# Optimization experiments

Hardware: AMD Instinct MI355X
Metric: run time of the kernel (lower is better)

## Reference

```python
import jax, jax.numpy as jnp
import numpy as np

H = 16          # num_heads
MAX_SCALE_MUL = float(np.log(100.0))
EPS = 1e-12     # F.normalize eps


def setup_inputs() -> dict:
    key = jax.random.key(0)
    ks = jax.random.split(key, 8)
    B, L, C = 8, 1024, 1024
    x = jax.random.normal(ks[0], (B, L, C), dtype=jnp.float32)
    attn_bias = jax.random.normal(ks[1], (1, H, L, L), dtype=jnp.float32) * 0.1
    w_qkv = jax.random.normal(ks[2], (3 * C, C), dtype=jnp.float32) * (C ** -0.5)
    q_bias = jnp.zeros((C,), dtype=jnp.float32)
    v_bias = jnp.zeros((C,), dtype=jnp.float32)
    scale_mul = jnp.full((1, H, 1, 1), np.log(4.0), dtype=jnp.float32)
    w_proj = jax.random.normal(ks[3], (C, C), dtype=jnp.float32) * (C ** -0.5)
    b_proj = jnp.zeros((C,), dtype=jnp.float32)
    return dict(x=x, attn_bias=attn_bias, w_qkv=w_qkv, q_bias=q_bias,
                v_bias=v_bias, scale_mul=scale_mul, w_proj=w_proj, b_proj=b_proj)


def _l2norm(t):
    # matches F.normalize(dim=-1): t / max(||t||_2, eps)
    n = jnp.sqrt(jnp.sum(t * t, axis=-1, keepdims=True))
    return t / jnp.maximum(n, EPS)


def reference(x, attn_bias, w_qkv, q_bias, v_bias, scale_mul, w_proj, b_proj):
    B, L, C = x.shape
    D = C // H
    bias = jnp.concatenate([q_bias, jnp.zeros_like(q_bias), v_bias])
    qkv = x @ w_qkv.T + bias                      # [B,L,3C]
    qkv = qkv.reshape(B, L, 3, H, D).transpose(2, 0, 3, 1, 4)  # [3,B,H,L,D]
    q, k, v = qkv[0], qkv[1], qkv[2]
    sm = jnp.exp(jnp.minimum(scale_mul, MAX_SCALE_MUL))        # [1,H,1,1]
    q = _l2norm(q) * sm
    k = _l2norm(k)
    attn = jnp.einsum('bhld,bhmd->bhlm', q, k) + attn_bias     # scale == 1
    attn = jax.nn.softmax(attn, axis=-1)
    out = jnp.einsum('bhlm,bhmd->bhld', attn, v)               # [B,H,L,D]
    out = out.transpose(0, 2, 1, 3).reshape(B, L, C)
    return out @ w_proj.T + b_proj
```

## Files before the change

### kernel.cpp

```cpp
#include <hip/hip_runtime.h>
#include <hip/hip_bf16.h>


#define LN100 4.6051701859880914f

typedef __attribute__((ext_vector_type(8))) short short8;
typedef __attribute__((ext_vector_type(4))) short short4v;
typedef __attribute__((ext_vector_type(4))) float f32x4;

#define MFMA_BF16(a, b, c) __builtin_amdgcn_mfma_f32_16x16x32_bf16(a, b, c, 0, 0, 0)

__device__ __forceinline__ unsigned short f2bf(float f) {
  unsigned u = __float_as_uint(f);
  u += 0x7fffu + ((u >> 16) & 1u);
  return (unsigned short)(u >> 16);
}
__device__ __forceinline__ float bf2f(unsigned short h) {
  return __uint_as_float(((unsigned)h) << 16);
}
__device__ __forceinline__ unsigned int pkbf2(float a, float b) {
  union { __hip_bfloat162 t; unsigned int u; } c;
  c.t = __float22bfloat162_rn(make_float2(a, b));
  return c.u;
}

__device__ __forceinline__ float bias_sel0(const float* qb, const float* vb, int col) {
  if (col < 1024) return qb[col];
  if (col < 2048) return 0.0f;
  return vb[col - 2048];
}

#define G2L16(gp, lp) __builtin_amdgcn_global_load_lds( \
    (const __attribute__((address_space(1))) void*)(gp), \
    (__attribute__((address_space(3))) void*)(lp), 16, 0, 0)

__global__ __launch_bounds__(256)
void split_f32_bf16(const float* __restrict__ in, unsigned short* __restrict__ hi,
                    unsigned short* __restrict__ lo, int n4)
{
  int i = blockIdx.x * blockDim.x + threadIdx.x;
  if (i >= n4) return;
  float4 v = ((const float4*)in)[i];
  ushort4 h, l;
  h.x = f2bf(v.x); l.x = f2bf(v.x - bf2f(h.x));
  h.y = f2bf(v.y); l.y = f2bf(v.y - bf2f(h.y));
  h.z = f2bf(v.z); l.z = f2bf(v.z - bf2f(h.z));
  h.w = f2bf(v.w); l.w = f2bf(v.w - bf2f(h.w));
  ((ushort4*)hi)[i] = h;
  ((ushort4*)lo)[i] = l;
}

template <int MODE>
__global__ __launch_bounds__(256)
void gemm_nt_split(const unsigned short* __restrict__ Ah, const unsigned short* __restrict__ Al,
                   const unsigned short* __restrict__ Wh, const unsigned short* __restrict__ Wl,
                   const float* __restrict__ b0, const float* __restrict__ b1,
                   float* __restrict__ C,
                   unsigned short* __restrict__ vth, unsigned short* __restrict__ vtl,
                   int M, int N, int K)
{
  __shared__ unsigned short sA[128 * 64];
  __shared__ unsigned short sW[128 * 64];

  const int tid  = threadIdx.x;
  const int lane = tid & 63;
  const int l15  = lane & 15, lg = lane >> 4;
  const int w    = tid >> 6;
  const int wr   = (w >> 1) << 6;
  const int wc   = (w & 1) << 6;
  const int m0   = blockIdx.y << 7;
  const int n0   = blockIdx.x << 7;

  f32x4 acc[4][4];
  #pragma unroll
  for (int i = 0; i < 4; ++i)
    #pragma unroll
    for (int j = 0; j < 4; ++j)
      acc[i][j] = (f32x4){0.f, 0.f, 0.f, 0.f};

  for (int k0 = 0; k0 < K; k0 += 32) {
    __syncthreads();
    #pragma unroll
    for (int u = 0; u < 4; ++u) {
      int idx = (u << 8) + tid;
      int row = idx >> 3;
      int c   = idx & 7;
      int s   = c ^ (row & 7);
      size_t rbA = (size_t)(m0 + row) * K + k0;
      size_t rbW = (size_t)(n0 + row) * K + k0;
      const unsigned short* srcA = (s < 4) ? (Ah + rbA + (s << 3))
                                           : (Al + rbA + ((s - 4) << 3));
      const unsigned short* srcW = (s < 4) ? (Wh + rbW + (s << 3))
                                           : (Wl + rbW + ((s - 4) << 3));
      G2L16(srcA, sA + (idx << 3));
      G2L16(srcW, sW + (idx << 3));
    }
    __syncthreads();

    short8 ah[4], al[4];
    #pragma unroll
    for (int i = 0; i < 4; ++i) {
      int row = wr + (i << 4) + l15;
      ah[i] = *(const short8*)(sA + (row << 6) + ((lg       ^ (row & 7)) << 3));
      al[i] = *(const short8*)(sA + (row << 6) + (((4 + lg) ^ (row & 7)) << 3));
    }
    #pragma unroll
    for (int j = 0; j < 4; ++j) {
      int row = wc + (j << 4) + l15;
      short8 wh = *(const short8*)(sW + (row << 6) + ((lg       ^ (row & 7)) << 3));
      short8 wl = *(const short8*)(sW + (row << 6) + (((4 + lg) ^ (row & 7)) << 3));
      #pragma unroll
      for (int i = 0; i < 4; ++i) {
        acc[i][j] = MFMA_BF16(ah[i], wh, acc[i][j]);
        acc[i][j] = MFMA_BF16(ah[i], wl, acc[i][j]);
        acc[i][j] = MFMA_BF16(al[i], wh, acc[i][j]);
      }
    }
  }

  if (MODE == 0 && n0 >= 2048) {
    #pragma unroll
    for (int j = 0; j < 4; ++j) {
      int col = n0 + wc + (j << 4) + l15;
      int d   = col - 2048;
      int hh  = d >> 6, dd = d & 63;
      float bb = b1[d];
      #pragma unroll
      for (int i = 0; i < 4; ++i) {
        int row  = m0 + wr + (i << 4) + (lg << 2);
        int bidx = row >> 10;
        int l    = row & 1023;
        size_t obase = ((((size_t)bidx << 4) + hh) << 6) + dd;
        obase = obase * 1024 + l;
        ushort4 hv, lv;
        float v0 = acc[i][j][0] + bb;
        float v1 = acc[i][j][1] + bb;
        float v2 = acc[i][j][2] + bb;
        float v3 = acc[i][j][3] + bb;
        hv.x = f2bf(v0); lv.x = f2bf(v0 - bf2f(hv.x));
        hv.y = f2bf(v1); lv.y = f2bf(v1 - bf2f(hv.y));
        hv.z = f2bf(v2); lv.z = f2bf(v2 - bf2f(hv.z));
        hv.w = f2bf(v3); lv.w = f2bf(v3 - bf2f(hv.w));
        *(ushort4*)(vth + obase) = hv;
        *(ushort4*)(vtl + obase) = lv;
      }
    }
  } else {
    #pragma unroll
    for (int j = 0; j < 4; ++j) {
      int col = n0 + wc + (j << 4) + l15;
      float bb = (MODE == 1) ? b0[col] : bias_sel0(b0, b1, col);
      #pragma unroll
      for (int i = 0; i < 4; ++i) {
        int rbase = m0 + wr + (i << 4) + (lg << 2);
        #pragma unroll
        for (int r = 0; r < 4; ++r)
          C[(size_t)(rbase + r) * N + col] = acc[i][j][r] + bb;
      }
    }
  }
}

__global__ __launch_bounds__(256)
void qk_norm_split(const float* __restrict__ qkv, const float* __restrict__ scale_mul,
                   unsigned short* __restrict__ qk_h, unsigned short* __restrict__ qk_l)
{
  int wave = (blockIdx.x << 2) + (threadIdx.x >> 6);
  int lane = threadIdx.x & 63;
  int h  = wave & 15;
  int bl = wave >> 4;
  size_t base = (size_t)bl * 3072 + (h << 6) + lane;
  float q = qkv[base];
  float k = qkv[base + 1024];
  float sq = q * q, sk = k * k;
  #pragma unroll
  for (int off = 32; off; off >>= 1) {
    sq += __shfl_xor(sq, off);
    sk += __shfl_xor(sk, off);
  }
  float sm = __expf(fminf(scale_mul[h], LN100));
  q = q / fmaxf(sqrtf(sq), 1e-12f) * sm;
  k = k / fmaxf(sqrtf(sk), 1e-12f);
  size_t ob = (size_t)bl * 2048 + (h << 6) + lane;
  unsigned short qh = f2bf(q);
  qk_h[ob] = qh;          qk_l[ob] = f2bf(q - bf2f(qh));
  unsigned short kh = f2bf(k);
  qk_h[ob + 1024] = kh;   qk_l[ob + 1024] = f2bf(k - bf2f(kh));
}

__global__ __launch_bounds__(256, 2)
void attn_mfma(const unsigned short* __restrict__ qk_h, const unsigned short* __restrict__ qk_l,
               const unsigned short* __restrict__ vth, const unsigned short* __restrict__ vtl,
               const float* __restrict__ bias,
               unsigned short* __restrict__ oh, unsigned short* __restrict__ ol)
{
  __shared__ unsigned short sKh[4096], sKl[4096];
  __shared__ unsigned short sVh[4096], sVl[4096];

  const int tid  = threadIdx.x;
  const int lane = tid & 63;
  const int l15  = lane & 15, lg = lane >> 4;
  const int w    = tid >> 6;
  const int qt = blockIdx.x & 7;
  const int h  = (blockIdx.x >> 3) & 15;
  const int b  = blockIdx.x >> 7;
  const int q0 = qt << 7;

  short8 qh[2][2], qlo[2][2];
  #pragma unroll
  for (int qf = 0; qf < 2; ++qf) {
    size_t rb = ((size_t)((b << 10) + q0 + (w << 5) + (qf << 4) + l15)) * 2048
              + (h << 6) + (lg << 3);
    qh[qf][0]  = *(const short8*)(qk_h + rb);
    qh[qf][1]  = *(const short8*)(qk_h + rb + 32);
    qlo[qf][0] = *(const short8*)(qk_l + rb);
    qlo[qf][1] = *(const short8*)(qk_l + rb + 32);
  }

  f32x4 ao[2][4];
  float mr[2], lr[2];
  #pragma unroll
  for (int qf = 0; qf < 2; ++qf) {
    #pragma unroll
    for (int j = 0; j < 4; ++j) ao[qf][j] = (f32x4){0.f, 0.f, 0.f, 0.f};
    mr[qf] = -3.0e38f; lr[qf] = 0.0f;
  }

  const unsigned short* kh_base = qk_h + 1024 + (h << 6);
  const unsigned short* kl_base = qk_l + 1024 + (h << 6);
  const size_t vbase = ((size_t)((b << 4) + h)) * 65536;
  const float* bias_base = bias + ((size_t)h << 20)
                         + (size_t)(q0 + (w << 5) + l15) * 1024 + (lg << 2);

  for (int kv0 = 0; kv0 < 1024; kv0 += 64) {
    __syncthreads();
    #pragma unroll
    for (int u = 0; u < 2; ++u) {
      int idx = (u << 8) + tid;
      int r = idx >> 3, c = idx & 7;
      int s = c ^ (r & 7);
      size_t krow = (size_t)((b << 10) + kv0 + r) * 2048 + (s << 3);
      size_t vrow = vbase + (size_t)r * 1024 + kv0 + (s << 3);
      G2L16(kh_base + krow, sKh + (idx << 3));
      G2L16(kl_base + krow, sKl + (idx << 3));
      G2L16(vth + vrow,     sVh + (idx << 3));
      G2L16(vtl + vrow,     sVl + (idx << 3));
    }
    float4 bb[2][4];
    #pragma unroll
    for (int qf = 0; qf < 2; ++qf)
      #pragma unroll
      for (int j = 0; j < 4; ++j)
        bb[qf][j] = *(const float4*)(bias_base + (size_t)(qf << 4) * 1024
                                     + kv0 + (j << 4));
    __syncthreads();

    f32x4 sv[2][4];
    #pragma unroll
    for (int j = 0; j < 4; ++j) {
      int row = (j << 4) + l15;
      int c0 = lg ^ (row & 7);
      int c1 = (lg + 4) ^ (row & 7);
      short8 kh0 = *(const short8*)(sKh + (row << 6) + (c0 << 3));
      short8 kl0 = *(const short8*)(sKl + (row << 6) + (c0 << 3));
      short8 kh1 = *(const short8*)(sKh + (row << 6) + (c1 << 3));
      short8 kl1 = *(const short8*)(sKl + (row << 6) + (c1 << 3));
      #pragma unroll
      for (int qf = 0; qf < 2; ++qf) {
        f32x4 a = (f32x4){0.f, 0.f, 0.f, 0.f};
        a = MFMA_BF16(kh0, qh[qf][0], a);
        a = MFMA_BF16(kl0, qh[qf][0], a);
        a = MFMA_BF16(kh0, qlo[qf][0], a);
        a = MFMA_BF16(kh1, qh[qf][1], a);
        a = MFMA_BF16(kl1, qh[qf][1], a);
        a = MFMA_BF16(kh1, qlo[qf][1], a);
        sv[qf][j] = a;
      }
    }

    unsigned int phw[2][8], plw[2][8];
    #pragma unroll
    for (int qf = 0; qf < 2; ++qf) {
      #pragma unroll
      for (int j = 0; j < 4; ++j) {
        sv[qf][j][0] += bb[qf][j].x;
        sv[qf][j][1] += bb[qf][j].y;
        sv[qf][j][2] += bb[qf][j].z;
        sv[qf][j][3] += bb[qf][j].w;
      }
      float mx = -3.0e38f;
      #pragma unroll
      for (int j = 0; j < 4; ++j)
        #pragma unroll
        for (int r = 0; r < 4; ++r) mx = fmaxf(mx, sv[qf][j][r]);
      mx = fmaxf(mx, __shfl_xor(mx, 16));
      mx = fmaxf(mx, __shfl_xor(mx, 32));
      float mn = fmaxf(mr[qf], mx);
      float al = __expf(mr[qf] - mn);
      mr[qf] = mn;
      float rs = 0.0f;
      #pragma unroll
      for (int j = 0; j < 4; ++j)
        #pragma unroll
        for (int r = 0; r < 4; ++r) {
          float e = __expf(sv[qf][j][r] - mn);
          sv[qf][j][r] = e;
          rs += e;
        }
      rs += __shfl_xor(rs, 16);
      rs += __shfl_xor(rs, 32);
      lr[qf] = lr[qf] * al + rs;
      #pragma unroll
      for (int r = 0; r < 4; ++r) {
        float av = __shfl(al, (lg << 2) + r);
        #pragma unroll
        for (int jd = 0; jd < 4; ++jd) ao[qf][jd][r] *= av;
      }
      #pragma unroll
      for (int j = 0; j < 4; ++j) {
        unsigned int h0 = pkbf2(sv[qf][j][0], sv[qf][j][1]);
        unsigned int h1 = pkbf2(sv[qf][j][2], sv[qf][j][3]);
        float r0 = sv[qf][j][0] - __uint_as_float(h0 << 16);
        float r1 = sv[qf][j][1] - __uint_as_float(h0 & 0xffff0000u);
        float r2 = sv[qf][j][2] - __uint_as_float(h1 << 16);
        float r3 = sv[qf][j][3] - __uint_as_float(h1 & 0xffff0000u);
        phw[qf][(j << 1)]     = h0;
        phw[qf][(j << 1) + 1] = h1;
        plw[qf][(j << 1)]     = pkbf2(r0, r1);
        plw[qf][(j << 1) + 1] = pkbf2(r2, r3);
      }
    }

    #pragma unroll
    for (int ks = 0; ks < 2; ++ks) {
      union { unsigned int w[4]; short8 v; } pa0, pa1, pl0, pl1;
      #pragma unroll
      for (int i = 0; i < 4; ++i) {
        pa0.w[i] = phw[0][(ks << 2) + i];
        pa1.w[i] = phw[1][(ks << 2) + i];
        pl0.w[i] = plw[0][(ks << 2) + i];
        pl1.w[i] = plw[1][(ks << 2) + i];
      }
      #pragma unroll
      for (int jd = 0; jd < 4; ++jd) {
        int vr  = (jd << 4) + l15;
        int c0  = ((ks << 2) + (lg >> 1))     ^ (vr & 7);
        int c1  = ((ks << 2) + 2 + (lg >> 1)) ^ (vr & 7);
        int sub = (lg & 1) << 2;
        short8 vh, vl;
        vh.lo = *(const short4v*)(sVh + (vr << 6) + (c0 << 3) + sub);
        vh.hi = *(const short4v*)(sVh + (vr << 6) + (c1 << 3) + sub);
        vl.lo = *(const short4v*)(sVl + (vr << 6) + (c0 << 3) + sub);
        vl.hi = *(const short4v*)(sVl + (vr << 6) + (c1 << 3) + sub);
        ao[0][jd] = MFMA_BF16(pa0.v, vh, ao[0][jd]);
        ao[0][jd] = MFMA_BF16(pa0.v, vl, ao[0][jd]);
        ao[0][jd] = MFMA_BF16(pl0.v, vh, ao[0][jd]);
        ao[1][jd] = MFMA_BF16(pa1.v, vh, ao[1][jd]);
        ao[1][jd] = MFMA_BF16(pa1.v, vl, ao[1][jd]);
        ao[1][jd] = MFMA_BF16(pl1.v, vh, ao[1][jd]);
      }
    }
  }

  #pragma unroll
  for (int qf = 0; qf < 2; ++qf)
    #pragma unroll
    for (int r = 0; r < 4; ++r) {
      float lv  = __shfl(lr[qf], (lg << 2) + r);
      float inv = 1.0f / lv;
      size_t orow = ((size_t)((b << 10) + q0 + (w << 5) + (qf << 4) + (lg << 2) + r)) * 1024
                  + (h << 6) + l15;
      #pragma unroll
      for (int jd = 0; jd < 4; ++jd) {
        float v = ao[qf][jd][r] * inv;
        unsigned short hb = f2bf(v);
        oh[orow + (jd << 4)] = hb;
        ol[orow + (jd << 4)] = f2bf(v - bf2f(hb));
      }
    }
}

template <int MODE>
__global__ __launch_bounds__(256)
void gemm_nt(const float* __restrict__ A, const float* __restrict__ Bw,
             const float* __restrict__ b0, const float* __restrict__ b1,
             float* __restrict__ C, int M, int N, int K)
{
  __shared__ float As[32][132];
  __shared__ float Bs[32][132];
  const int tid = threadIdx.x;
  const int tx = tid & 15, ty = tid >> 4;
  const int m0 = blockIdx.y << 7;
  const int n0 = blockIdx.x << 7;

  float acc[8][8];
  #pragma unroll
  for (int i = 0; i < 8; ++i)
    #pragma unroll
    for (int j = 0; j < 8; ++j) acc[i][j] = 0.0f;

  for (int k0 = 0; k0 < K; k0 += 32) {
    #pragma unroll
    for (int u = 0; u < 4; ++u) {
      int f   = tid + (u << 8);
      int row = f >> 3;
      int kk  = (f & 7) << 2;
      float4 av = *(const float4*)(A  + (size_t)(m0 + row) * K + k0 + kk);
      As[kk + 0][row] = av.x; As[kk + 1][row] = av.y;
      As[kk + 2][row] = av.z; As[kk + 3][row] = av.w;
      float4 bv = *(const float4*)(Bw + (size_t)(n0 + row) * K + k0 + kk);
      Bs[kk + 0][row] = bv.x; Bs[kk + 1][row] = bv.y;
      Bs[kk + 2][row] = bv.z; Bs[kk + 3][row] = bv.w;
    }
    __syncthreads();
    #pragma unroll
    for (int kk = 0; kk < 32; ++kk) {
      float a[8], bq[8];
      *(float4*)(a)      = *(const float4*)(&As[kk][(ty << 3)]);
      *(float4*)(a + 4)  = *(const float4*)(&As[kk][(ty << 3) + 4]);
      *(float4*)(bq)     = *(const float4*)(&Bs[kk][(tx << 3)]);
      *(float4*)(bq + 4) = *(const float4*)(&Bs[kk][(tx << 3) + 4]);
      #pragma unroll
      for (int i = 0; i < 8; ++i)
        #pragma unroll
        for (int j = 0; j < 8; ++j)
          acc[i][j] = fmaf(a[i], bq[j], acc[i][j]);
    }
    __syncthreads();
  }

  #pragma unroll
  for (int i = 0; i < 8; ++i) {
    int row = m0 + (ty << 3) + i;
    #pragma unroll
    for (int j4 = 0; j4 < 2; ++j4) {
      int col = n0 + (tx << 3) + (j4 << 2);
      float4 r;
      float bbv[4];
      #pragma unroll
      for (int j = 0; j < 4; ++j)
        bbv[j] = (MODE == 0) ? bias_sel0(b0, b1, col + j) : b0[col + j];
      r.x = acc[i][j4 * 4 + 0] + bbv[0];
      r.y = acc[i][j4 * 4 + 1] + bbv[1];
      r.z = acc[i][j4 * 4 + 2] + bbv[2];
      r.w = acc[i][j4 * 4 + 3] + bbv[3];
      *(float4*)(C + (size_t)row * N + col) = r;
    }
  }
}

__global__ __launch_bounds__(256)
void qk_norm(float* __restrict__ qkv, const float* __restrict__ scale_mul)
{
  int wave = (blockIdx.x << 2) + (threadIdx.x >> 6);
  int lane = threadIdx.x & 63;
  int h  = wave & 15;
  int bl = wave >> 4;
  size_t base = (size_t)bl * 3072 + (h << 6) + lane;
  float q = qkv[base];
  float k = qkv[base + 1024];
  float sq = q * q, sk = k * k;
  #pragma unroll
  for (int off = 32; off; off >>= 1) {
    sq += __shfl_xor(sq, off);
    sk += __shfl_xor(sk, off);
  }
  float sm = __expf(fminf(scale_mul[h], LN100));
  q = q / fmaxf(sqrtf(sq), 1e-12f) * sm;
  k = k / fmaxf(sqrtf(sk), 1e-12f);
  qkv[base]        = q;
  qkv[base + 1024] = k;
}

#define SW(r, c4) ((((c4) ^ ((r) >> 2)) & 15) << 2)

template <int OUTMODE>
__global__ __launch_bounds__(256)
void attn_fwd(const float* __restrict__ qkv, const float* __restrict__ bias,
              float* __restrict__ aout,
              unsigned short* __restrict__ ah, unsigned short* __restrict__ al)
{
  __shared__ float Qs[64][64];
  __shared__ float Ks[64][64];
  __shared__ float Vs[64][64];
  __shared__ float Ps[64][64];

  const int tid = threadIdx.x;
  const int tx = tid & 15, ty = tid >> 4;
  const int qt = blockIdx.x & 15;
  const int h  = (blockIdx.x >> 4) & 15;
  const int b  = blockIdx.x >> 8;
  const int q0 = qt << 6;

  #pragma unroll
  for (int u = 0; u < 4; ++u) {
    int f = tid + (u << 8);
    int r = f >> 4, c4 = f & 15;
    float4 v = *(const float4*)(qkv + (size_t)(b * 1024 + q0 + r) * 3072 + (h << 6) + (c4 << 2));
    *(float4*)(&Qs[r][SW(r, c4)]) = v;
  }

  float o[4][4];
  float mr[4], lr[4];
  #pragma unroll
  for (int i = 0; i < 4; ++i) {
    mr[i] = -3.0e38f; lr[i] = 0.0f;
    #pragma unroll
    for (int j = 0; j < 4; ++j) o[i][j] = 0.0f;
  }

  for (int kv0 = 0; kv0 < 1024; kv0 += 64) {
    __syncthreads();
    #pragma unroll
    for (int u = 0; u < 4; ++u) {
      int f = tid + (u << 8);
      int r = f >> 4, c4 = f & 15;
      size_t gb = (size_t)(b * 1024 + kv0 + r) * 3072 + (h << 6) + (c4 << 2);
      *(float4*)(&Ks[r][SW(r, c4)]) = *(const float4*)(qkv + gb + 1024);
      *(float4*)(&Vs[r][SW(r, c4)]) = *(const float4*)(qkv + gb + 2048);
    }
    __syncthreads();

    float s[4][4];
    #pragma unroll
    for (int i = 0; i < 4; ++i)
      #pragma unroll
      for (int j = 0; j < 4; ++j) s[i][j] = 0.0f;

    #pragma unroll 4
    for (int d4 = 0; d4 < 16; ++d4) {
      float4 qv[4], kv[4];
      #pragma unroll
      for (int i = 0; i < 4; ++i)
        qv[i] = *(const float4*)(&Qs[(ty << 2) + i][SW((ty << 2) + i, d4)]);
      #pragma unroll
      for (int j = 0; j < 4; ++j)
        kv[j] = *(const float4*)(&Ks[(tx << 2) + j][SW((tx << 2) + j, d4)]);
      #pragma unroll
      for (int i = 0; i < 4; ++i)
        #pragma unroll
        for (int j = 0; j < 4; ++j)
          s[i][j] += qv[i].x * kv[j].x + qv[i].y * kv[j].y +
                     qv[i].z * kv[j].z + qv[i].w * kv[j].w;
    }

    float p[4][4];
    #pragma unroll
    for (int i = 0; i < 4; ++i) {
      float4 bv = *(const float4*)(bias + (size_t)((h << 10) + q0 + (ty << 2) + i) * 1024
                                        + kv0 + (tx << 2));
      s[i][0] += bv.x; s[i][1] += bv.y; s[i][2] += bv.z; s[i][3] += bv.w;
      float mx = fmaxf(fmaxf(s[i][0], s[i][1]), fmaxf(s[i][2], s[i][3]));
      #pragma unroll
      for (int off = 1; off < 16; off <<= 1) mx = fmaxf(mx, __shfl_xor(mx, off));
      float mn = fmaxf(mr[i], mx);
      float alp = __expf(mr[i] - mn);
      float rs = 0.0f;
      #pragma unroll
      for (int j = 0; j < 4; ++j) { p[i][j] = __expf(s[i][j] - mn); rs += p[i][j]; }
      #pragma unroll
      for (int off = 1; off < 16; off <<= 1) rs += __shfl_xor(rs, off);
      lr[i] = lr[i] * alp + rs;
      mr[i] = mn;
      #pragma unroll
      for (int j = 0; j < 4; ++j) o[i][j] *= alp;
    }

    #pragma unroll
    for (int jj = 0; jj < 4; ++jj)
      #pragma unroll
      for (int i = 0; i < 4; ++i)
        Ps[(tx << 2) + jj][SW((tx << 2) + jj, ty) + i] = p[i][jj];
    __syncthreads();

    #pragma unroll 8
    for (int j = 0; j < 64; ++j) {
      float4 pv = *(const float4*)(&Ps[j][SW(j, ty)]);
      float4 vv = *(const float4*)(&Vs[j][SW(j, tx)]);
      o[0][0] += pv.x * vv.x; o[0][1] += pv.x * vv.y; o[0][2] += pv.x * vv.z; o[0][3] += pv.x * vv.w;
      o[1][0] += pv.y * vv.x; o[1][1] += pv.y * vv.y; o[1][2] += pv.y * vv.z; o[1][3] += pv.y * vv.w;
      o[2][0] += pv.z * vv.x; o[2][1] += pv.z * vv.y; o[2][2] += pv.z * vv.z; o[2][3] += pv.z * vv.w;
      o[3][0] += pv.w * vv.x; o[3][1] += pv.w * vv.y; o[3][2] += pv.w * vv.z; o[3][3] += pv.w * vv.w;
    }
  }

  #pragma unroll
  for (int i = 0; i < 4; ++i) {
    float inv = 1.0f / lr[i];
    float v0 = o[i][0] * inv, v1 = o[i][1] * inv, v2 = o[i][2] * inv, v3 = o[i][3] * inv;
    if (OUTMODE == 0) {
      float4 r; r.x = v0; r.y = v1; r.z = v2; r.w = v3;
      *(float4*)(aout + (size_t)(b * 1024 + q0 + (ty << 2) + i) * 1024 + (h << 6) + (tx << 2)) = r;
    } else {
      ushort4 hh, ll;
      hh.x = f2bf(v0); ll.x = f2bf(v0 - bf2f(hh.x));
      hh.y = f2bf(v1); ll.y = f2bf(v1 - bf2f(hh.y));
      hh.z = f2bf(v2); ll.z = f2bf(v2 - bf2f(hh.z));
      hh.w = f2bf(v3); ll.w = f2bf(v3 - bf2f(hh.w));
      size_t idx = (size_t)(b * 1024 + q0 + (ty << 2) + i) * 256 + (h << 4) + tx;
      ((ushort4*)ah)[idx] = hh;
      ((ushort4*)al)[idx] = ll;
    }
  }
}

extern "C" void kernel_launch(void* const* d_in, const int* in_sizes, int n_in,
                              void* d_out, int out_size, void* d_ws, size_t ws_size,
                              hipStream_t stream) {
  const float* x         = (const float*)d_in[0];
  const float* attn_bias = (const float*)d_in[1];
  const float* w_qkv     = (const float*)d_in[2];
  const float* q_bias    = (const float*)d_in[3];
  const float* v_bias    = (const float*)d_in[4];
  const float* scale_mul = (const float*)d_in[5];
  const float* w_proj    = (const float*)d_in[6];
  const float* b_proj    = (const float*)d_in[7];
  float* out = (float*)d_out;

  const size_t MiB = 1024 * 1024;
  char* ws = (char*)d_ws;
  dim3 blk(256);

  if (ws_size >= 240 * MiB) {
    float*          qkv = (float*)ws;
    unsigned short* xh  = (unsigned short*)(ws + 96  * MiB);
    unsigned short* xl  = (unsigned short*)(ws + 112 * MiB);
    unsigned short* qkh = (unsigned short*)(ws + 128 * MiB);
    unsigned short* qkl = (unsigned short*)(ws + 160 * MiB);
    unsigned short* vth = (unsigned short*)(ws + 192 * MiB);
    unsigned short* vtl = (unsigned short*)(ws + 208 * MiB);
    unsigned short* wqh = (unsigned short*)(ws + 224 * MiB);
    unsigned short* wql = (unsigned short*)(ws + 230 * MiB);
    unsigned short* wph = (unsigned short*)(ws + 236 * MiB);
    unsigned short* wpl = (unsigned short*)(ws + 238 * MiB);

    split_f32_bf16<<<dim3(8192), blk, 0, stream>>>(x,      xh,  xl,  2097152);
    split_f32_bf16<<<dim3(3072), blk, 0, stream>>>(w_qkv,  wqh, wql, 786432);
    split_f32_bf16<<<dim3(1024), blk, 0, stream>>>(w_proj, wph, wpl, 262144);

    gemm_nt_split<0><<<dim3(24, 64), blk, 0, stream>>>(xh, xl, wqh, wql,
        q_bias, v_bias, qkv, vth, vtl, 8192, 3072, 1024);
    qk_norm_split<<<dim3(32768), blk, 0, stream>>>(qkv, scale_mul, qkh, qkl);
    attn_mfma<<<dim3(1024), blk, 0, stream>>>(qkh, qkl, vth, vtl, attn_bias, xh, xl);
    gemm_nt_split<1><<<dim3(8, 64), blk, 0, stream>>>(xh, xl, wph, wpl,
        b_proj, nullptr, out, nullptr, nullptr, 8192, 1024, 1024);
  } else if (ws_size >= 144 * MiB) {
    float*          qkv = (float*)ws;
    unsigned short* xh  = (unsigned short*)(ws + 96  * MiB);
    unsigned short* xl  = (unsigned short*)(ws + 112 * MiB);
    unsigned short* wqh = (unsigned short*)(ws + 128 * MiB);
    unsigned short* wql = (unsigned short*)(ws + 134 * MiB);
    unsigned short* wph = (unsigned short*)(ws + 140 * MiB);
    unsigned short* wpl = (unsigned short*)(ws + 142 * MiB);

    split_f32_bf16<<<dim3(8192), blk, 0, stream>>>(x,      xh,  xl,  2097152);
    split_f32_bf16<<<dim3(3072), blk, 0, stream>>>(w_qkv,  wqh, wql, 786432);
    split_f32_bf16<<<dim3(1024), blk, 0, stream>>>(w_proj, wph, wpl, 262144);

    gemm_nt_split<2><<<dim3(24, 64), blk, 0, stream>>>(xh, xl, wqh, wql,
        q_bias, v_bias, qkv, nullptr, nullptr, 8192, 3072, 1024);
    qk_norm<<<dim3(32768), blk, 0, stream>>>(qkv, scale_mul);
    attn_fwd<1><<<dim3(2048), blk, 0, stream>>>(qkv, attn_bias, nullptr, xh, xl);
    gemm_nt_split<1><<<dim3(8, 64), blk, 0, stream>>>(xh, xl, wph, wpl,
        b_proj, nullptr, out, nullptr, nullptr, 8192, 1024, 1024);
  } else {
    float* qkv = (float*)ws;
    float* att = qkv + (size_t)8192 * 3072;
    gemm_nt<0><<<dim3(24, 64), blk, 0, stream>>>(x, w_qkv, q_bias, v_bias, qkv, 8192, 3072, 1024);
    qk_norm<<<dim3(32768), blk, 0, stream>>>(qkv, scale_mul);
    attn_fwd<0><<<dim3(2048), blk, 0, stream>>>(qkv, attn_bias, att, nullptr, nullptr);
    gemm_nt<1><<<dim3(8, 64), blk, 0, stream>>>(att, w_proj, b_proj, nullptr, out, 8192, 1024, 1024);
  }
}
```

Baseline: 540.9 us.

## Permute V-transpose layout so PV operands load as single 16-byte LDS reads

The QKV GEMM epilogue now writes V-transposed with a permuted key index, so each lane's PV B-operand lives in one contiguous 8-element chunk. The attention kernel then reads V with one short8 LDS load per hi/lo instead of two short4 halves. The attention bias is now fed in as the initial MFMA accumulator rather than added afterwards. The per-qf loop is also restructured so QK, softmax and PV run one q-fragment at a time, which cuts live registers (sv and the packed P arrays) but reloads the K fragments from LDS for each qf.

```diff
diff --git a/kernel.cpp b/kernel.cpp
--- a/kernel.cpp
+++ b/kernel.cpp
@@ -5,8 +5,8 @@
 #define LN100 4.6051701859880914f
 
 typedef __attribute__((ext_vector_type(8))) short short8;
-typedef __attribute__((ext_vector_type(4))) short short4v;
 typedef __attribute__((ext_vector_type(4))) float f32x4;
+typedef __attribute__((ext_vector_type(4))) unsigned int u32x4;
 
 #define MFMA_BF16(a, b, c) __builtin_amdgcn_mfma_f32_16x16x32_bf16(a, b, c, 0, 0, 0)
 
@@ -130,8 +130,9 @@
         int row  = m0 + wr + (i << 4) + (lg << 2);
         int bidx = row >> 10;
         int l    = row & 1023;
+        int cbase = (((l >> 4) & 1) << 2) + (((l >> 2) & 3) << 3) + ((l >> 5) << 5);
         size_t obase = ((((size_t)bidx << 4) + hh) << 6) + dd;
-        obase = obase * 1024 + l;
+        obase = obase * 1024 + cbase;
         ushort4 hv, lv;
         float v0 = acc[i][j][0] + bb;
         float v1 = acc[i][j][1] + bb;
@@ -246,53 +247,37 @@
       G2L16(vth + vrow,     sVh + (idx << 3));
       G2L16(vtl + vrow,     sVl + (idx << 3));
     }
-    float4 bb[2][4];
-    #pragma unroll
-    for (int qf = 0; qf < 2; ++qf)
-      #pragma unroll
-      for (int j = 0; j < 4; ++j)
-        bb[qf][j] = *(const float4*)(bias_base + (size_t)(qf << 4) * 1024
+    __syncthreads();
+
+    #pragma unroll
+    for (int qf = 0; qf < 2; ++qf) {
+      f32x4 sv[4];
+      #pragma unroll
+      for (int j = 0; j < 4; ++j) {
+        float4 bv = *(const float4*)(bias_base + (size_t)(qf << 4) * 1024
                                      + kv0 + (j << 4));
-    __syncthreads();
-
-    f32x4 sv[2][4];
-    #pragma unroll
-    for (int j = 0; j < 4; ++j) {
-      int row = (j << 4) + l15;
-      int c0 = lg ^ (row & 7);
-      int c1 = (lg + 4) ^ (row & 7);
-      short8 kh0 = *(const short8*)(sKh + (row << 6) + (c0 << 3));
-      short8 kl0 = *(const short8*)(sKl + (row << 6) + (c0 << 3));
-      short8 kh1 = *(const short8*)(sKh + (row << 6) + (c1 << 3));
-      short8 kl1 = *(const short8*)(sKl + (row << 6) + (c1 << 3));
-      #pragma unroll
-      for (int qf = 0; qf < 2; ++qf) {
-        f32x4 a = (f32x4){0.f, 0.f, 0.f, 0.f};
+        f32x4 a = (f32x4){bv.x, bv.y, bv.z, bv.w};
+        int row = (j << 4) + l15;
+        int c0 = lg ^ (row & 7);
+        int c1 = (lg + 4) ^ (row & 7);
+        short8 kh0 = *(const short8*)(sKh + (row << 6) + (c0 << 3));
+        short8 kl0 = *(const short8*)(sKl + (row << 6) + (c0 << 3));
+        short8 kh1 = *(const short8*)(sKh + (row << 6) + (c1 << 3));
+        short8 kl1 = *(const short8*)(sKl + (row << 6) + (c1 << 3));
         a = MFMA_BF16(kh0, qh[qf][0], a);
         a = MFMA_BF16(kl0, qh[qf][0], a);
         a = MFMA_BF16(kh0, qlo[qf][0], a);
         a = MFMA_BF16(kh1, qh[qf][1], a);
         a = MFMA_BF16(kl1, qh[qf][1], a);
         a = MFMA_BF16(kh1, qlo[qf][1], a);
-        sv[qf][j] = a;
+        sv[j] = a;
       }
-    }
-
-    unsigned int phw[2][8], plw[2][8];
-    #pragma unroll
-    for (int qf = 0; qf < 2; ++qf) {
-      #pragma unroll
-      for (int j = 0; j < 4; ++j) {
-        sv[qf][j][0] += bb[qf][j].x;
-        sv[qf][j][1] += bb[qf][j].y;
-        sv[qf][j][2] += bb[qf][j].z;
-        sv[qf][j][3] += bb[qf][j].w;
-      }
+
       float mx = -3.0e38f;
       #pragma unroll
       for (int j = 0; j < 4; ++j)
         #pragma unroll
-        for (int r = 0; r < 4; ++r) mx = fmaxf(mx, sv[qf][j][r]);
+        for (int r = 0; r < 4; ++r) mx = fmaxf(mx, sv[j][r]);
       mx = fmaxf(mx, __shfl_xor(mx, 16));
       mx = fmaxf(mx, __shfl_xor(mx, 32));
       float mn = fmaxf(mr[qf], mx);
@@ -303,8 +288,8 @@
       for (int j = 0; j < 4; ++j)
         #pragma unroll
         for (int r = 0; r < 4; ++r) {
-          float e = __expf(sv[qf][j][r] - mn);
-          sv[qf][j][r] = e;
+          float e = __expf(sv[j][r] - mn);
+          sv[j][r] = e;
           rs += e;
         }
       rs += __shfl_xor(rs, 16);
@@ -316,48 +301,34 @@
         #pragma unroll
         for (int jd = 0; jd < 4; ++jd) ao[qf][jd][r] *= av;
       }
-      #pragma unroll
-      for (int j = 0; j < 4; ++j) {
-        unsigned int h0 = pkbf2(sv[qf][j][0], sv[qf][j][1]);
-        unsigned int h1 = pkbf2(sv[qf][j][2], sv[qf][j][3]);
-        float r0 = sv[qf][j][0] - __uint_as_float(h0 << 16);
-        float r1 = sv[qf][j][1] - __uint_as_float(h0 & 0xffff0000u);
-        float r2 = sv[qf][j][2] - __uint_as_float(h1 << 16);
-        float r3 = sv[qf][j][3] - __uint_as_float(h1 & 0xffff0000u);
-        phw[qf][(j << 1)]     = h0;
-        phw[qf][(j << 1) + 1] = h1;
-        plw[qf][(j << 1)]     = pkbf2(r0, r1);
-        plw[qf][(j << 1) + 1] = pkbf2(r2, r3);
-      }
-    }
-
-    #pragma unroll
-    for (int ks = 0; ks < 2; ++ks) {
-      union { unsigned int w[4]; short8 v; } pa0, pa1, pl0, pl1;
-      #pragma unroll
-      for (int i = 0; i < 4; ++i) {
-        pa0.w[i] = phw[0][(ks << 2) + i];
-        pa1.w[i] = phw[1][(ks << 2) + i];
-        pl0.w[i] = plw[0][(ks << 2) + i];
-        pl1.w[i] = plw[1][(ks << 2) + i];
-      }
-      #pragma unroll
-      for (int jd = 0; jd < 4; ++jd) {
-        int vr  = (jd << 4) + l15;
-        int c0  = ((ks << 2) + (lg >> 1))     ^ (vr & 7);
-        int c1  = ((ks << 2) + 2 + (lg >> 1)) ^ (vr & 7);
-        int sub = (lg & 1) << 2;
-        short8 vh, vl;
-        vh.lo = *(const short4v*)(sVh + (vr << 6) + (c0 << 3) + sub);
-        vh.hi = *(const short4v*)(sVh + (vr << 6) + (c1 << 3) + sub);
-        vl.lo = *(const short4v*)(sVl + (vr << 6) + (c0 << 3) + sub);
-        vl.hi = *(const short4v*)(sVl + (vr << 6) + (c1 << 3) + sub);
-        ao[0][jd] = MFMA_BF16(pa0.v, vh, ao[0][jd]);
-        ao[0][jd] = MFMA_BF16(pa0.v, vl, ao[0][jd]);
-        ao[0][jd] = MFMA_BF16(pl0.v, vh, ao[0][jd]);
-        ao[1][jd] = MFMA_BF16(pa1.v, vh, ao[1][jd]);
-        ao[1][jd] = MFMA_BF16(pa1.v, vl, ao[1][jd]);
-        ao[1][jd] = MFMA_BF16(pl1.v, vh, ao[1][jd]);
+
+      #pragma unroll
+      for (int ks = 0; ks < 2; ++ks) {
+        unsigned int h0 = pkbf2(sv[2*ks][0],     sv[2*ks][1]);
+        unsigned int h1 = pkbf2(sv[2*ks][2],     sv[2*ks][3]);
+        unsigned int h2 = pkbf2(sv[2*ks + 1][0], sv[2*ks + 1][1]);
+        unsigned int h3 = pkbf2(sv[2*ks + 1][2], sv[2*ks + 1][3]);
+        unsigned int l0 = pkbf2(sv[2*ks][0]     - __uint_as_float(h0 << 16),
+                                sv[2*ks][1]     - __uint_as_float(h0 & 0xffff0000u));
+        unsigned int l1 = pkbf2(sv[2*ks][2]     - __uint_as_float(h1 << 16),
+                                sv[2*ks][3]     - __uint_as_float(h1 & 0xffff0000u));
+        unsigned int l2 = pkbf2(sv[2*ks + 1][0] - __uint_as_float(h2 << 16),
+                                sv[2*ks + 1][1] - __uint_as_float(h2 & 0xffff0000u));
+        unsigned int l3 = pkbf2(sv[2*ks + 1][2] - __uint_as_float(h3 << 16),
+                                sv[2*ks + 1][3] - __uint_as_float(h3 & 0xffff0000u));
+        union { u32x4 u; short8 s; } ph, pl;
+        ph.u = (u32x4){h0, h1, h2, h3};
+        pl.u = (u32x4){l0, l1, l2, l3};
+        #pragma unroll
+        for (int jd = 0; jd < 4; ++jd) {
+          int vr = (jd << 4) + l15;
+          int c  = ((ks << 2) + lg) ^ (vr & 7);
+          short8 vh = *(const short8*)(sVh + (vr << 6) + (c << 3));
+          short8 vl = *(const short8*)(sVl + (vr << 6) + (c << 3));
+          ao[qf][jd] = MFMA_BF16(ph.s, vh, ao[qf][jd]);
+          ao[qf][jd] = MFMA_BF16(ph.s, vl, ao[qf][jd]);
+          ao[qf][jd] = MFMA_BF16(pl.s, vh, ao[qf][jd]);
+        }
       }
     }
   }
```

Result: no change. 539.1 us (-0.3%).
